# Optimization experiments

Measured on AMD Instinct MI355X. Metric: run time of the kernel, lower is better.

The kernel has to match this reference:

```python
import jax, jax.numpy as jnp
import numpy as np

N = 50000          # nodes
E_RAND = 800000    # random edges
E = E_RAND + N     # + self loops -> 850000
F_IN = 256         # nembed
F_HID = 64         # nhid
H = 8              # nheads
NCLASS = 40
ALPHA = 0.2        # leakyrelu slope


def setup_inputs() -> dict:
    key = jax.random.key(0)
    ks = jax.random.split(key, 8)
    x = jax.random.normal(ks[0], (N, F_IN), dtype=jnp.float32)
    # random edges + self loops (guarantees every row-sum > 0, like adj + I)
    er = jax.random.randint(ks[1], (2, E_RAND), 0, N, dtype=jnp.int32)
    loops = jnp.tile(jnp.arange(N, dtype=jnp.int32)[None, :], (2, 1))
    edge_index = jnp.concatenate([er, loops], axis=1)  # [2, E]
    # per-head attention params (xavier-ish scale)
    W = jax.random.normal(ks[2], (H, F_IN, F_HID), dtype=jnp.float32) * (1.0 / np.sqrt(F_IN))
    a = jax.random.normal(ks[3], (H, 2 * F_HID), dtype=jnp.float32) * 0.1
    Wo = jax.random.normal(ks[4], (H * F_HID, F_HID), dtype=jnp.float32) * (1.0 / np.sqrt(H * F_HID))
    ao = jax.random.normal(ks[5], (2 * F_HID,), dtype=jnp.float32) * 0.1
    mlp_w = jax.random.normal(ks[6], (NCLASS, F_HID), dtype=jnp.float32) * 0.05
    mlp_b = jnp.zeros((NCLASS,), dtype=jnp.float32)
    return {"x": x, "edge_index": edge_index, "W": W, "a": a,
            "Wo": Wo, "ao": ao, "mlp_w": mlp_w, "mlp_b": mlp_b}


def _leaky(v):
    return jnp.where(v > 0, v, ALPHA * v)


def _spgat_layer(x, W, a, src, dst, n):
    """pyGAT SpGraphAttentionLayer (eval mode, dropout = identity).
    out[i] = sum_{e: src=i} exp(-leakyrelu(a.[h_src;h_dst])) * h[dst] / rowsum_i
    """
    h = x @ W                         # [N, D]
    D = W.shape[1]
    s_src = h @ a[:D]                 # [N]
    s_dst = h @ a[D:]                 # [N]
    # per-edge unnormalized attention (note the -exp(leaky) of original sp impl)
    e = jnp.exp(-_leaky(s_src[src] + s_dst[dst]))          # [E]
    rowsum = jax.ops.segment_sum(e, src, num_segments=n)   # [N]
    num = jax.ops.segment_sum(e[:, None] * h[dst], src, num_segments=n)  # [N, D]
    return num / rowsum[:, None]


def reference(x, edge_index, W, a, Wo, ao, mlp_w, mlp_b):
    src, dst = edge_index[0], edge_index[1]
    # multi-head attention, concat=True -> elu inside each head
    heads = [jax.nn.elu(_spgat_layer(x, W[i], a[i], src, dst, N)) for i in range(H)]
    xc = jnp.concatenate(heads, axis=1)                     # [N, H*F_HID]
    # dropout (eval) = identity
    xo = jax.nn.elu(_spgat_layer(xc, Wo, ao, src, dst, N))  # [N, F_HID]
    return xo @ mlp_w.T + mlp_b                             # [N, NCLASS]
```

## Files before the change

### kernel.cpp

```cpp
#include <hip/hip_runtime.h>

#define NN 50000
#define HH 8
#define ALPHA 0.2f
#define NPAD 50048

typedef short short8 __attribute__((ext_vector_type(8)));
typedef float f32x4 __attribute__((ext_vector_type(4)));

__device__ __forceinline__ float elu_f(float x) {
  return x > 0.f ? x : __expf(x) - 1.f;
}

__device__ __forceinline__ unsigned short f2bf(float f) {
  unsigned int u = __float_as_uint(f);
  unsigned int r = (u + 0x7fffu + ((u >> 16) & 1u)) >> 16;
  return (unsigned short)r;
}

__global__ void cvt_all_kernel(const float* __restrict__ x, unsigned short* __restrict__ xb,
                               const float* __restrict__ W, unsigned short* __restrict__ Wt,
                               const float* __restrict__ Wo, unsigned short* __restrict__ Wot,
                               int n4x) {
  int tid = blockIdx.x * 256 + threadIdx.x;
  if (tid < n4x) {
    float4 v = ((const float4*)x)[tid];
    ushort4 o;
    o.x = f2bf(v.x); o.y = f2bf(v.y); o.z = f2bf(v.z); o.w = f2bf(v.w);
    ((ushort4*)xb)[tid] = o;
    return;
  }
  int t1 = tid - n4x;
  if (t1 < HH * 256 * 64) {
    int h = t1 / (256 * 64);
    int rem = t1 - h * 256 * 64;
    int k = rem >> 6, c = rem & 63;
    Wt[((size_t)h * 64 + c) * 256 + k] = f2bf(W[t1]);
    return;
  }
  int t2 = t1 - HH * 256 * 64;
  if (t2 < 512 * 64) {
    int k = t2 >> 6, c = t2 & 63;
    Wot[(size_t)c * 512 + k] = f2bf(Wo[t2]);
  }
}

__global__ void hist_kernel(const int* __restrict__ src, int* __restrict__ cnt, int E) {
  int e = blockIdx.x * blockDim.x + threadIdx.x;
  if (e < E) atomicAdd(&cnt[src[e]], 1);
}

__global__ __launch_bounds__(1024) void scan_blocks_kernel(const int* __restrict__ cnt,
    int* __restrict__ tmp, int* __restrict__ bsum, int n) {
  __shared__ int sh[1024];
  int i = blockIdx.x * 1024 + threadIdx.x;
  int v = (i < n) ? cnt[i] : 0;
  sh[threadIdx.x] = v;
  __syncthreads();
  for (int off = 1; off < 1024; off <<= 1) {
    int t = (threadIdx.x >= off) ? sh[threadIdx.x - off] : 0;
    __syncthreads();
    sh[threadIdx.x] += t;
    __syncthreads();
  }
  if (i < n) tmp[i] = sh[threadIdx.x] - v;
  if (threadIdx.x == 1023) bsum[blockIdx.x] = sh[1023];
}

__global__ __launch_bounds__(64) void scan_top_kernel(const int* __restrict__ bsum,
    int* __restrict__ boffs, int nb) {
  int L = threadIdx.x;
  int v = (L < nb) ? bsum[L] : 0;
  int incl = v;
#pragma unroll
  for (int off = 1; off < 64; off <<= 1) {
    int t = __shfl_up(incl, off, 64);
    if (L >= off) incl += t;
  }
  if (L < nb) boffs[L] = incl - v;
}

__global__ __launch_bounds__(1024) void scan_apply_kernel(const int* __restrict__ tmp,
    const int* __restrict__ boffs, int* __restrict__ row_ptr, int* __restrict__ nxt,
    int n, int E) {
  int i = blockIdx.x * 1024 + threadIdx.x;
  if (i < n) {
    int s = tmp[i] + boffs[blockIdx.x];
    row_ptr[i] = s;
    nxt[i] = s;
  }
  if (i == 0) row_ptr[n] = E;
}

__global__ void scatter_kernel(const int* __restrict__ src, const int* __restrict__ dst,
                               int* __restrict__ nxt, int* __restrict__ col, int E) {
  int e = blockIdx.x * blockDim.x + threadIdx.x;
  if (e < E) {
    int p = atomicAdd(&nxt[src[e]], 1);
    col[p] = dst[e];
  }
}

__global__ __launch_bounds__(256) void mfma_gemm1_kernel(
    const unsigned short* __restrict__ A, const unsigned short* __restrict__ Bt,
    const float* __restrict__ Aatt, unsigned short* __restrict__ Cout,
    float* __restrict__ ss, float* __restrict__ sd, int N) {
  __shared__ unsigned short Bs[64][264];
  int w = threadIdx.x >> 6, L = threadIdx.x & 63;
  int quad = L >> 4, l16 = L & 15;
  int m0 = blockIdx.x * 64;
  int myrow = m0 + w * 16 + l16;

  const unsigned short* Ar = A + (size_t)myrow * 256 + quad * 8;
  short8 areg[8];
#pragma unroll
  for (int ks = 0; ks < 8; ++ks) areg[ks] = *(const short8*)(Ar + ks * 32);

  for (int y = 0; y < HH; ++y) {
    __syncthreads();
    {
      const unsigned short* Bsrc = Bt + (size_t)y * 64 * 256;
      for (int c = threadIdx.x; c < 2048; c += 256) {
        int n = c >> 5;
        int kq = (c & 31) << 3;
        *(uint4*)&Bs[n][kq] = *(const uint4*)(Bsrc + (size_t)n * 256 + kq);
      }
    }
    __syncthreads();

    f32x4 acc[4];
#pragma unroll
    for (int nt = 0; nt < 4; ++nt) acc[nt] = (f32x4)(0.f);
#pragma unroll
    for (int ks = 0; ks < 8; ++ks) {
#pragma unroll
      for (int nt = 0; nt < 4; ++nt) {
        short8 b = *(const short8*)&Bs[l16 + 16 * nt][ks * 32 + quad * 8];
        acc[nt] = __builtin_amdgcn_mfma_f32_16x16x32_bf16(areg[ks], b, acc[nt], 0, 0, 0);
      }
    }

    float as[4], ad[4];
#pragma unroll
    for (int nt = 0; nt < 4; ++nt) {
      as[nt] = Aatt[y * 128 + l16 + 16 * nt];
      ad[nt] = Aatt[y * 128 + 64 + l16 + 16 * nt];
    }
#pragma unroll
    for (int reg = 0; reg < 4; ++reg) {
      float p = 0.f, q = 0.f;
#pragma unroll
      for (int nt = 0; nt < 4; ++nt) {
        p += acc[nt][reg] * as[nt];
        q += acc[nt][reg] * ad[nt];
      }
#pragma unroll
      for (int off = 1; off < 16; off <<= 1) {
        p += __shfl_xor(p, off, 64);
        q += __shfl_xor(q, off, 64);
      }
      int row = m0 + w * 16 + quad * 4 + reg;
      if (l16 == 0 && row < N) {
        ss[(size_t)row * 8 + y] = p;
        sd[(size_t)row * 8 + y] = q;
      }
    }
#pragma unroll
    for (int reg = 0; reg < 4; ++reg) {
      int row = m0 + w * 16 + quad * 4 + reg;
      if (row < N) {
#pragma unroll
        for (int nt = 0; nt < 4; ++nt)
          Cout[(size_t)row * 512 + y * 64 + l16 + 16 * nt] = f2bf(acc[nt][reg]);
      }
    }
  }
}

__global__ __launch_bounds__(256) void mfma_gemm2_kernel(
    const unsigned short* __restrict__ A, const unsigned short* __restrict__ Bt,
    const float* __restrict__ Aatt, unsigned short* __restrict__ Cout,
    float* __restrict__ ss, float* __restrict__ sd, int N) {
  __shared__ unsigned short Bs[64][520];
  {
    for (int c = threadIdx.x; c < 4096; c += 256) {
      int n = c >> 6;
      int kq = (c & 63) << 3;
      *(uint4*)&Bs[n][kq] = *(const uint4*)(Bt + (size_t)n * 512 + kq);
    }
  }
  __syncthreads();

  int w = threadIdx.x >> 6, L = threadIdx.x & 63;
  int quad = L >> 4, l16 = L & 15;
  int m0 = blockIdx.x * 64;
  int myrow = m0 + w * 16 + l16;
  const unsigned short* Ar = A + (size_t)myrow * 512 + quad * 8;

  f32x4 acc[4];
#pragma unroll
  for (int nt = 0; nt < 4; ++nt) acc[nt] = (f32x4)(0.f);

  short8 a_cur = *(const short8*)(Ar);
  for (int k0 = 0; k0 < 512; k0 += 32) {
    short8 a_nxt;
    if (k0 + 32 < 512) a_nxt = *(const short8*)(Ar + k0 + 32);
#pragma unroll
    for (int nt = 0; nt < 4; ++nt) {
      short8 b = *(const short8*)&Bs[l16 + 16 * nt][k0 + quad * 8];
      acc[nt] = __builtin_amdgcn_mfma_f32_16x16x32_bf16(a_cur, b, acc[nt], 0, 0, 0);
    }
    a_cur = a_nxt;
  }

  float as[4], ad[4];
#pragma unroll
  for (int nt = 0; nt < 4; ++nt) {
    as[nt] = Aatt[l16 + 16 * nt];
    ad[nt] = Aatt[64 + l16 + 16 * nt];
  }
#pragma unroll
  for (int reg = 0; reg < 4; ++reg) {
    float p = 0.f, q = 0.f;
#pragma unroll
    for (int nt = 0; nt < 4; ++nt) {
      p += acc[nt][reg] * as[nt];
      q += acc[nt][reg] * ad[nt];
    }
#pragma unroll
    for (int off = 1; off < 16; off <<= 1) {
      p += __shfl_xor(p, off, 64);
      q += __shfl_xor(q, off, 64);
    }
    int row = m0 + w * 16 + quad * 4 + reg;
    if (l16 == 0 && row < N) { ss[row] = p; sd[row] = q; }
  }
#pragma unroll
  for (int reg = 0; reg < 4; ++reg) {
    int row = m0 + w * 16 + quad * 4 + reg;
    if (row < N) {
#pragma unroll
      for (int nt = 0; nt < 4; ++nt)
        Cout[(size_t)row * 64 + l16 + 16 * nt] = f2bf(acc[nt][reg]);
    }
  }
}

__global__ __launch_bounds__(256) void agg1_kernel(const unsigned short* __restrict__ table,
    const float* __restrict__ ss, const float* __restrict__ sd,
    const int* __restrict__ row_ptr, const int* __restrict__ col,
    unsigned short* __restrict__ xc, int N) {
  int wid = threadIdx.x >> 6, L = threadIdx.x & 63;
  int n = blockIdx.x * 4 + wid;
  if (n >= N) return;
  int h = L >> 3;
  int b = L & 7;
  int srcsel = h << 3;
  float ssn = ss[n * 8 + h];
  int k0 = row_ptr[n], deg = row_ptr[n + 1] - k0;
  float acc[8];
#pragma unroll
  for (int t = 0; t < 8; ++t) acc[t] = 0.f;
  float rs = 0.f;

  for (int c0 = 0; c0 < deg; c0 += 64) {
    int j = c0 + L;
    int d_l = (j < deg) ? col[k0 + j] : 0;
    int m = min(64, deg - c0);
    for (int g = 0; g < m; g += 8) {
      int eoff = g + b;
      int de = __shfl(d_l, eoff, 64);
      float s = ssn + sd[(size_t)de * 8 + h];
      float e = __expf(-fmaxf(s, ALPHA * s));
      if (eoff >= m) e = 0.f;
      rs += e;
      int gm = min(8, m - g);
      uint4 rv[8];
#pragma unroll
      for (int t = 0; t < 8; ++t) {
        if (t < gm) {
          int dg = __builtin_amdgcn_readlane(d_l, g + t);
          rv[t] = *((const uint4*)(table + (size_t)dg * 512) + L);
        }
      }
#pragma unroll
      for (int t = 0; t < 8; ++t) {
        if (t < gm) {
          float ew = __shfl(e, srcsel + t, 64);
          const unsigned int* up = (const unsigned int*)&rv[t];
#pragma unroll
          for (int v = 0; v < 4; ++v) {
            acc[2 * v]     += ew * __uint_as_float(up[v] << 16);
            acc[2 * v + 1] += ew * __uint_as_float(up[v] & 0xffff0000u);
          }
        }
      }
    }
  }
  rs += __shfl_xor(rs, 1, 64);
  rs += __shfl_xor(rs, 2, 64);
  rs += __shfl_xor(rs, 4, 64);
  float inv = 1.f / rs;
  short8 pk;
#pragma unroll
  for (int t = 0; t < 8; ++t) pk[t] = (short)f2bf(elu_f(acc[t] * inv));
  *(short8*)(xc + (size_t)n * 512 + L * 8) = pk;
}

__global__ __launch_bounds__(256) void agg2_kernel(const unsigned short* __restrict__ table,
    const float* __restrict__ ss, const float* __restrict__ sd,
    const int* __restrict__ row_ptr, const int* __restrict__ col,
    float* __restrict__ xo, int N) {
  int wid = threadIdx.x >> 6, L = threadIdx.x & 63;
  int n = blockIdx.x * 4 + wid;
  if (n >= N) return;
  float ssn = ss[n];
  int k0 = row_ptr[n], deg = row_ptr[n + 1] - k0;
  float acc = 0.f, rs = 0.f;
  const char* base = (const char*)table;

  for (int c0 = 0; c0 < deg; c0 += 64) {
    int j = c0 + L;
    int d_l = 0;
    float e_l = 0.f;
    if (j < deg) {
      d_l = col[k0 + j];
      float s = ssn + sd[d_l];
      e_l = __expf(-fmaxf(s, ALPHA * s));
    }
    rs += e_l;
    int m = min(64, deg - c0);
    int off_l = d_l << 7;
    for (int g = 0; g < m; g += 8) {
      int gm = min(8, m - g);
      unsigned hv[8];
#pragma unroll
      for (int t = 0; t < 8; ++t) {
        if (t < gm) {
          int so = __builtin_amdgcn_readlane(off_l, g + t);
          hv[t] = *(const unsigned short*)(base + so + L * 2);
        }
      }
#pragma unroll
      for (int t = 0; t < 8; ++t) {
        if (t < gm) {
          float ew = __uint_as_float(
              (unsigned)__builtin_amdgcn_readlane(__float_as_uint(e_l), g + t));
          acc += ew * __uint_as_float(hv[t] << 16);
        }
      }
    }
  }
#pragma unroll
  for (int off = 1; off < 64; off <<= 1) rs += __shfl_xor(rs, off, 64);
  xo[(size_t)n * 64 + L] = elu_f(acc / rs);
}

__global__ __launch_bounds__(256) void final_kernel(const float* __restrict__ xo,
    const float* __restrict__ mlp_w, const float* __restrict__ mlp_b,
    float* __restrict__ out, int total) {
  __shared__ float wsh[40 * 65];
  __shared__ float bsh[40];
  for (int i = threadIdx.x; i < 40 * 64; i += 256) wsh[(i >> 6) * 65 + (i & 63)] = mlp_w[i];
  if (threadIdx.x < 40) bsh[threadIdx.x] = mlp_b[threadIdx.x];
  __syncthreads();
  int idx = blockIdx.x * 256 + threadIdx.x;
  if (idx >= total) return;
  int n = idx / 40, c = idx - n * 40;
  const float* xr = xo + (size_t)n * 64;
  const float* wr = wsh + c * 65;
  float acc = bsh[c];
#pragma unroll
  for (int j = 0; j < 64; ++j) acc += xr[j] * wr[j];
  out[idx] = acc;
}

extern "C" void kernel_launch(void* const* d_in, const int* in_sizes, int n_in,
                              void* d_out, int out_size, void* d_ws, size_t ws_size,
                              hipStream_t stream) {
  (void)n_in; (void)out_size; (void)ws_size;
  const float* x  = (const float*)d_in[0];
  const int*   ei = (const int*)d_in[1];
  const float* W  = (const float*)d_in[2];
  const float* a  = (const float*)d_in[3];
  const float* Wo = (const float*)d_in[4];
  const float* ao = (const float*)d_in[5];
  const float* mw = (const float*)d_in[6];
  const float* mb = (const float*)d_in[7];
  float* out = (float*)d_out;

  const int N = NN;
  const int E = in_sizes[1] / 2;
  const int* src = ei;
  const int* dst = ei + E;

  char* ws = (char*)d_ws;
  size_t off = 0;
  auto alloc = [&](size_t bytes) {
    char* p = ws + off;
    off = (off + bytes + 255) & ~(size_t)255;
    return p;
  };
  unsigned short* xb  = (unsigned short*)alloc((size_t)NPAD * 256 * 2);
  unsigned short* Wt  = (unsigned short*)alloc((size_t)HH * 64 * 256 * 2);
  unsigned short* Wot = (unsigned short*)alloc((size_t)64 * 512 * 2);
  unsigned short* h1b = (unsigned short*)alloc((size_t)N * 512 * 2);
  float* ss1     = (float*)alloc((size_t)N * 8 * 4);
  float* sd1     = (float*)alloc((size_t)N * 8 * 4);
  unsigned short* xc = (unsigned short*)alloc((size_t)NPAD * 512 * 2);
  unsigned short* h2b = (unsigned short*)alloc((size_t)N * 64 * 2);
  float* ss2     = (float*)alloc((size_t)N * 4);
  float* sd2     = (float*)alloc((size_t)N * 4);
  float* xo      = (float*)alloc((size_t)N * 64 * 4);
  int*   row_ptr = (int*)  alloc((size_t)(N + 1) * 4);
  int*   nxt     = (int*)  alloc((size_t)N * 4);
  int*   cnt     = (int*)  alloc((size_t)N * 4);
  int*   tmp     = (int*)  alloc((size_t)N * 4);
  int*   bsum    = (int*)  alloc(64 * 4);
  int*   boffs   = (int*)  alloc(64 * 4);
  int*   colv    = (int*)  alloc((size_t)E * 4);

  int eb = (E + 255) / 256;
  int nb1024 = (N + 1023) / 1024;
  int n4x = N * 256 / 4;
  int cvt_total = n4x + HH * 256 * 64 + 512 * 64;

  hipLaunchKernelGGL(cvt_all_kernel, dim3((cvt_total + 255) / 256), dim3(256), 0, stream,
                     x, xb, W, Wt, Wo, Wot, n4x);

  hipMemsetAsync(cnt, 0, (size_t)N * 4, stream);
  hipLaunchKernelGGL(hist_kernel, dim3(eb), dim3(256), 0, stream, src, cnt, E);
  hipLaunchKernelGGL(scan_blocks_kernel, dim3(nb1024), dim3(1024), 0, stream, cnt, tmp, bsum, N);
  hipLaunchKernelGGL(scan_top_kernel, dim3(1), dim3(64), 0, stream, bsum, boffs, nb1024);
  hipLaunchKernelGGL(scan_apply_kernel, dim3(nb1024), dim3(1024), 0, stream, tmp, boffs, row_ptr, nxt, N, E);
  hipLaunchKernelGGL(scatter_kernel, dim3(eb), dim3(256), 0, stream, src, dst, nxt, colv, E);

  hipLaunchKernelGGL(mfma_gemm1_kernel, dim3(NPAD / 64), dim3(256), 0, stream,
                     xb, Wt, a, h1b, ss1, sd1, N);
  hipLaunchKernelGGL(agg1_kernel, dim3((N + 3) / 4), dim3(256), 0, stream,
                     h1b, ss1, sd1, row_ptr, colv, xc, N);

  hipLaunchKernelGGL(mfma_gemm2_kernel, dim3(NPAD / 64), dim3(256), 0, stream,
                     xc, Wot, ao, h2b, ss2, sd2, N);
  hipLaunchKernelGGL(agg2_kernel, dim3((N + 3) / 4), dim3(256), 0, stream,
                     h2b, ss2, sd2, row_ptr, colv, xo, N);

  hipLaunchKernelGGL(final_kernel, dim3((N * 40 + 255) / 256), dim3(256), 0, stream,
                     xo, mw, mb, out, N * 40);
}
```

Baseline: 457.2 us.

## Fuse x bf16 conversion into GEMM1, split agg1 heads, fuse agg2 with MLP

The separate fp32-to-bf16 conversion of x is removed: GEMM1 now reads fp32 rows directly and converts them in registers, which avoids writing and re-reading the bf16 copy. agg1 is split into two blocks per node group, each covering four heads with 8-byte gathers and 16 edges per step. The block index is interleaved so the two halves of a node group run close together. agg2 is fused with the final MLP through shared memory, which drops the xo round trip and one launch. The cost is more blocks and more edge-weight recomputation in agg1, and a per-block reload of the MLP weights into shared memory.

```diff
diff --git a/kernel.cpp b/kernel.cpp
--- a/kernel.cpp
+++ b/kernel.cpp
@@ -18,27 +18,17 @@
   return (unsigned short)r;
 }
 
-__global__ void cvt_all_kernel(const float* __restrict__ x, unsigned short* __restrict__ xb,
-                               const float* __restrict__ W, unsigned short* __restrict__ Wt,
-                               const float* __restrict__ Wo, unsigned short* __restrict__ Wot,
-                               int n4x) {
+__global__ void cvt_w_kernel(const float* __restrict__ W, unsigned short* __restrict__ Wt,
+                             const float* __restrict__ Wo, unsigned short* __restrict__ Wot) {
   int tid = blockIdx.x * 256 + threadIdx.x;
-  if (tid < n4x) {
-    float4 v = ((const float4*)x)[tid];
-    ushort4 o;
-    o.x = f2bf(v.x); o.y = f2bf(v.y); o.z = f2bf(v.z); o.w = f2bf(v.w);
-    ((ushort4*)xb)[tid] = o;
+  if (tid < HH * 256 * 64) {
+    int h = tid / (256 * 64);
+    int rem = tid - h * 256 * 64;
+    int k = rem >> 6, c = rem & 63;
+    Wt[((size_t)h * 64 + c) * 256 + k] = f2bf(W[tid]);
     return;
   }
-  int t1 = tid - n4x;
-  if (t1 < HH * 256 * 64) {
-    int h = t1 / (256 * 64);
-    int rem = t1 - h * 256 * 64;
-    int k = rem >> 6, c = rem & 63;
-    Wt[((size_t)h * 64 + c) * 256 + k] = f2bf(W[t1]);
-    return;
-  }
-  int t2 = t1 - HH * 256 * 64;
+  int t2 = tid - HH * 256 * 64;
   if (t2 < 512 * 64) {
     int k = t2 >> 6, c = t2 & 63;
     Wot[(size_t)c * 512 + k] = f2bf(Wo[t2]);
@@ -102,7 +92,7 @@
 }
 
 __global__ __launch_bounds__(256) void mfma_gemm1_kernel(
-    const unsigned short* __restrict__ A, const unsigned short* __restrict__ Bt,
+    const float* __restrict__ X, const unsigned short* __restrict__ Bt,
     const float* __restrict__ Aatt, unsigned short* __restrict__ Cout,
     float* __restrict__ ss, float* __restrict__ sd, int N) {
   __shared__ unsigned short Bs[64][264];
@@ -110,11 +100,19 @@
   int quad = L >> 4, l16 = L & 15;
   int m0 = blockIdx.x * 64;
   int myrow = m0 + w * 16 + l16;
-
-  const unsigned short* Ar = A + (size_t)myrow * 256 + quad * 8;
+  int rowc = min(myrow, N - 1);
+
+  const float* Ar = X + (size_t)rowc * 256 + quad * 8;
   short8 areg[8];
 #pragma unroll
-  for (int ks = 0; ks < 8; ++ks) areg[ks] = *(const short8*)(Ar + ks * 32);
+  for (int ks = 0; ks < 8; ++ks) {
+    float4 a0 = *(const float4*)(Ar + ks * 32);
+    float4 a1 = *(const float4*)(Ar + ks * 32 + 4);
+    areg[ks][0] = (short)f2bf(a0.x); areg[ks][1] = (short)f2bf(a0.y);
+    areg[ks][2] = (short)f2bf(a0.z); areg[ks][3] = (short)f2bf(a0.w);
+    areg[ks][4] = (short)f2bf(a1.x); areg[ks][5] = (short)f2bf(a1.y);
+    areg[ks][6] = (short)f2bf(a1.z); areg[ks][7] = (short)f2bf(a1.w);
+  }
 
   for (int y = 0; y < HH; ++y) {
     __syncthreads();
@@ -250,49 +248,50 @@
     const float* __restrict__ ss, const float* __restrict__ sd,
     const int* __restrict__ row_ptr, const int* __restrict__ col,
     unsigned short* __restrict__ xc, int N) {
+  int bid = blockIdx.x;
+  int r8 = bid & 7;
+  int p = r8 >> 2;
+  int nb = ((bid >> 3) << 2) | (r8 & 3);
   int wid = threadIdx.x >> 6, L = threadIdx.x & 63;
-  int n = blockIdx.x * 4 + wid;
+  int n = nb * 4 + wid;
   if (n >= N) return;
-  int h = L >> 3;
-  int b = L & 7;
-  int srcsel = h << 3;
+  int hq = L >> 4;
+  int h = p * 4 + hq;
+  int el = L & 15;
   float ssn = ss[n * 8 + h];
   int k0 = row_ptr[n], deg = row_ptr[n + 1] - k0;
-  float acc[8];
-#pragma unroll
-  for (int t = 0; t < 8; ++t) acc[t] = 0.f;
+  float acc[4] = {0.f, 0.f, 0.f, 0.f};
   float rs = 0.f;
+  const char* tb = (const char*)table + p * 512;
 
   for (int c0 = 0; c0 < deg; c0 += 64) {
     int j = c0 + L;
     int d_l = (j < deg) ? col[k0 + j] : 0;
     int m = min(64, deg - c0);
-    for (int g = 0; g < m; g += 8) {
-      int eoff = g + b;
+    for (int g = 0; g < m; g += 16) {
+      int eoff = g + el;
       int de = __shfl(d_l, eoff, 64);
       float s = ssn + sd[(size_t)de * 8 + h];
       float e = __expf(-fmaxf(s, ALPHA * s));
       if (eoff >= m) e = 0.f;
       rs += e;
-      int gm = min(8, m - g);
-      uint4 rv[8];
-#pragma unroll
-      for (int t = 0; t < 8; ++t) {
+      int gm = min(16, m - g);
+      uint2 rv[16];
+#pragma unroll
+      for (int t = 0; t < 16; ++t) {
         if (t < gm) {
           int dg = __builtin_amdgcn_readlane(d_l, g + t);
-          rv[t] = *((const uint4*)(table + (size_t)dg * 512) + L);
+          rv[t] = *(const uint2*)(tb + (size_t)dg * 1024 + L * 8);
         }
       }
 #pragma unroll
-      for (int t = 0; t < 8; ++t) {
+      for (int t = 0; t < 16; ++t) {
         if (t < gm) {
-          float ew = __shfl(e, srcsel + t, 64);
-          const unsigned int* up = (const unsigned int*)&rv[t];
-#pragma unroll
-          for (int v = 0; v < 4; ++v) {
-            acc[2 * v]     += ew * __uint_as_float(up[v] << 16);
-            acc[2 * v + 1] += ew * __uint_as_float(up[v] & 0xffff0000u);
-          }
+          float ew = __shfl(e, (hq << 4) + t, 64);
+          acc[0] += ew * __uint_as_float(rv[t].x << 16);
+          acc[1] += ew * __uint_as_float(rv[t].x & 0xffff0000u);
+          acc[2] += ew * __uint_as_float(rv[t].y << 16);
+          acc[3] += ew * __uint_as_float(rv[t].y & 0xffff0000u);
         }
       }
     }
@@ -300,79 +299,83 @@
   rs += __shfl_xor(rs, 1, 64);
   rs += __shfl_xor(rs, 2, 64);
   rs += __shfl_xor(rs, 4, 64);
+  rs += __shfl_xor(rs, 8, 64);
   float inv = 1.f / rs;
-  short8 pk;
-#pragma unroll
-  for (int t = 0; t < 8; ++t) pk[t] = (short)f2bf(elu_f(acc[t] * inv));
-  *(short8*)(xc + (size_t)n * 512 + L * 8) = pk;
-}
-
-__global__ __launch_bounds__(256) void agg2_kernel(const unsigned short* __restrict__ table,
+  ushort4 pk;
+  pk.x = f2bf(elu_f(acc[0] * inv));
+  pk.y = f2bf(elu_f(acc[1] * inv));
+  pk.z = f2bf(elu_f(acc[2] * inv));
+  pk.w = f2bf(elu_f(acc[3] * inv));
+  *(ushort4*)(xc + (size_t)n * 512 + p * 256 + L * 4) = pk;
+}
+
+__global__ __launch_bounds__(256) void agg2_final_kernel(const unsigned short* __restrict__ table,
     const float* __restrict__ ss, const float* __restrict__ sd,
     const int* __restrict__ row_ptr, const int* __restrict__ col,
-    float* __restrict__ xo, int N) {
-  int wid = threadIdx.x >> 6, L = threadIdx.x & 63;
-  int n = blockIdx.x * 4 + wid;
-  if (n >= N) return;
-  float ssn = ss[n];
-  int k0 = row_ptr[n], deg = row_ptr[n + 1] - k0;
-  float acc = 0.f, rs = 0.f;
-  const char* base = (const char*)table;
-
-  for (int c0 = 0; c0 < deg; c0 += 64) {
-    int j = c0 + L;
-    int d_l = 0;
-    float e_l = 0.f;
-    if (j < deg) {
-      d_l = col[k0 + j];
-      float s = ssn + sd[d_l];
-      e_l = __expf(-fmaxf(s, ALPHA * s));
-    }
-    rs += e_l;
-    int m = min(64, deg - c0);
-    int off_l = d_l << 7;
-    for (int g = 0; g < m; g += 8) {
-      int gm = min(8, m - g);
-      unsigned hv[8];
-#pragma unroll
-      for (int t = 0; t < 8; ++t) {
-        if (t < gm) {
-          int so = __builtin_amdgcn_readlane(off_l, g + t);
-          hv[t] = *(const unsigned short*)(base + so + L * 2);
-        }
-      }
-#pragma unroll
-      for (int t = 0; t < 8; ++t) {
-        if (t < gm) {
-          float ew = __uint_as_float(
-              (unsigned)__builtin_amdgcn_readlane(__float_as_uint(e_l), g + t));
-          acc += ew * __uint_as_float(hv[t] << 16);
-        }
-      }
-    }
-  }
-#pragma unroll
-  for (int off = 1; off < 64; off <<= 1) rs += __shfl_xor(rs, off, 64);
-  xo[(size_t)n * 64 + L] = elu_f(acc / rs);
-}
-
-__global__ __launch_bounds__(256) void final_kernel(const float* __restrict__ xo,
     const float* __restrict__ mlp_w, const float* __restrict__ mlp_b,
-    float* __restrict__ out, int total) {
+    float* __restrict__ out, int N) {
   __shared__ float wsh[40 * 65];
   __shared__ float bsh[40];
+  __shared__ float osh[4][68];
   for (int i = threadIdx.x; i < 40 * 64; i += 256) wsh[(i >> 6) * 65 + (i & 63)] = mlp_w[i];
   if (threadIdx.x < 40) bsh[threadIdx.x] = mlp_b[threadIdx.x];
   __syncthreads();
-  int idx = blockIdx.x * 256 + threadIdx.x;
-  if (idx >= total) return;
-  int n = idx / 40, c = idx - n * 40;
-  const float* xr = xo + (size_t)n * 64;
-  const float* wr = wsh + c * 65;
-  float acc = bsh[c];
-#pragma unroll
-  for (int j = 0; j < 64; ++j) acc += xr[j] * wr[j];
-  out[idx] = acc;
+
+  int wid = threadIdx.x >> 6, L = threadIdx.x & 63;
+  int n = blockIdx.x * 4 + wid;
+  bool act = (n < N);
+  float o = 0.f;
+  if (act) {
+    float ssn = ss[n];
+    int k0 = row_ptr[n], deg = row_ptr[n + 1] - k0;
+    float acc = 0.f, rs = 0.f;
+    const char* base = (const char*)table;
+    for (int c0 = 0; c0 < deg; c0 += 64) {
+      int j = c0 + L;
+      int d_l = 0;
+      float e_l = 0.f;
+      if (j < deg) {
+        d_l = col[k0 + j];
+        float s = ssn + sd[d_l];
+        e_l = __expf(-fmaxf(s, ALPHA * s));
+      }
+      rs += e_l;
+      int m = min(64, deg - c0);
+      int off_l = d_l << 7;
+      for (int g = 0; g < m; g += 8) {
+        int gm = min(8, m - g);
+        unsigned hv[8];
+#pragma unroll
+        for (int t = 0; t < 8; ++t) {
+          if (t < gm) {
+            int so = __builtin_amdgcn_readlane(off_l, g + t);
+            hv[t] = *(const unsigned short*)(base + so + L * 2);
+          }
+        }
+#pragma unroll
+        for (int t = 0; t < 8; ++t) {
+          if (t < gm) {
+            float ew = __uint_as_float(
+                (unsigned)__builtin_amdgcn_readlane(__float_as_uint(e_l), g + t));
+            acc += ew * __uint_as_float(hv[t] << 16);
+          }
+        }
+      }
+    }
+#pragma unroll
+    for (int off = 1; off < 64; off <<= 1) rs += __shfl_xor(rs, off, 64);
+    o = elu_f(acc / rs);
+  }
+  osh[wid][L] = o;
+  __syncthreads();
+  if (act && L < 40) {
+    const float* wr = wsh + L * 65;
+    const float* orow = osh[wid];
+    float acc = bsh[L];
+#pragma unroll
+    for (int j = 0; j < 64; ++j) acc += orow[j] * wr[j];
+    out[(size_t)n * 40 + L] = acc;
+  }
 }
 
 extern "C" void kernel_launch(void* const* d_in, const int* in_sizes, int n_in,
@@ -401,7 +404,6 @@
     off = (off + bytes + 255) & ~(size_t)255;
     return p;
   };
-  unsigned short* xb  = (unsigned short*)alloc((size_t)NPAD * 256 * 2);
   unsigned short* Wt  = (unsigned short*)alloc((size_t)HH * 64 * 256 * 2);
   unsigned short* Wot = (unsigned short*)alloc((size_t)64 * 512 * 2);
   unsigned short* h1b = (unsigned short*)alloc((size_t)N * 512 * 2);
@@ -411,7 +413,6 @@
   unsigned short* h2b = (unsigned short*)alloc((size_t)N * 64 * 2);
   float* ss2     = (float*)alloc((size_t)N * 4);
   float* sd2     = (float*)alloc((size_t)N * 4);
-  float* xo      = (float*)alloc((size_t)N * 64 * 4);
   int*   row_ptr = (int*)  alloc((size_t)(N + 1) * 4);
   int*   nxt     = (int*)  alloc((size_t)N * 4);
   int*   cnt     = (int*)  alloc((size_t)N * 4);
@@ -422,11 +423,9 @@
 
   int eb = (E + 255) / 256;
   int nb1024 = (N + 1023) / 1024;
-  int n4x = N * 256 / 4;
-  int cvt_total = n4x + HH * 256 * 64 + 512 * 64;
-
-  hipLaunchKernelGGL(cvt_all_kernel, dim3((cvt_total + 255) / 256), dim3(256), 0, stream,
-                     x, xb, W, Wt, Wo, Wot, n4x);
+
+  hipLaunchKernelGGL(cvt_w_kernel, dim3((HH * 256 * 64 + 512 * 64 + 255) / 256), dim3(256),
+                     0, stream, W, Wt, Wo, Wot);
 
   hipMemsetAsync(cnt, 0, (size_t)N * 4, stream);
   hipLaunchKernelGGL(hist_kernel, dim3(eb), dim3(256), 0, stream, src, cnt, E);
@@ -436,15 +435,12 @@
   hipLaunchKernelGGL(scatter_kernel, dim3(eb), dim3(256), 0, stream, src, dst, nxt, colv, E);
 
   hipLaunchKernelGGL(mfma_gemm1_kernel, dim3(NPAD / 64), dim3(256), 0, stream,
-                     xb, Wt, a, h1b, ss1, sd1, N);
-  hipLaunchKernelGGL(agg1_kernel, dim3((N + 3) / 4), dim3(256), 0, stream,
+                     x, Wt, a, h1b, ss1, sd1, N);
+  hipLaunchKernelGGL(agg1_kernel, dim3(2 * ((N + 3) / 4)), dim3(256), 0, stream,
                      h1b, ss1, sd1, row_ptr, colv, xc, N);
 
   hipLaunchKernelGGL(mfma_gemm2_kernel, dim3(NPAD / 64), dim3(256), 0, stream,
                      xc, Wot, ao, h2b, ss2, sd2, N);
-  hipLaunchKernelGGL(agg2_kernel, dim3((N + 3) / 4), dim3(256), 0, stream,
-                     h2b, ss2, sd2, row_ptr, colv, xo, N);
-
-  hipLaunchKernelGGL(final_kernel, dim3((N * 40 + 255) / 256), dim3(256), 0, stream,
-                     xo, mw, mb, out, N * 40);
-}
+  hipLaunchKernelGGL(agg2_final_kernel, dim3((N + 3) / 4), dim3(256), 0, stream,
+                     h2b, ss2, sd2, row_ptr, colv, mw, mb, out, N);
+}
```

Result: faster. 441.4 us (-3.5%).
